# Kernel tuning notes

Measured on AMD Instinct MI355X. Metric: run time of the kernel, lower is better.

Reference implementation:

```python
import jax, jax.numpy as jnp
import numpy as np

H = 64  # lstm_units
FORGET_BIAS = 1.0  # TF LSTMCell default


def setup_inputs() -> dict:
    key = jax.random.key(0)
    k1, k2, k3 = jax.random.split(key, 3)
    B, T = 256, 2048
    x = jax.random.normal(k1, (B, T, 1), dtype=jnp.float32)
    # Layer 1: LSTMCell(64), input dim 1 -> kernel [(1+64), 4*64]
    W1 = jax.random.normal(k2, (1 + H, 4 * H), dtype=jnp.float32) * 0.1
    b1 = jnp.zeros((4 * H,), dtype=jnp.float32)
    # Layer 2: LSTMCell(1), input dim 64 -> kernel [(64+1), 4*1]
    W2 = jax.random.normal(k3, (H + 1, 4), dtype=jnp.float32) * 0.1
    b2 = jnp.zeros((4,), dtype=jnp.float32)
    return {"x": x, "W1": W1, "b1": b1, "W2": W2, "b2": b2}


def _lstm_step(c, h, xt, W, b):
    # TF LSTMCell: gates from concat([x, h]) @ W + b, order i, j, f, o
    z = jnp.concatenate([xt, h], axis=-1) @ W + b
    i, j, f, o = jnp.split(z, 4, axis=-1)
    c_new = jax.nn.sigmoid(f + FORGET_BIAS) * c + jax.nn.sigmoid(i) * jnp.tanh(j)
    h_new = jax.nn.sigmoid(o) * jnpp_tanh(c_new) if False else jax.nn.sigmoid(o) * jnp.tanh(c_new)
    return c_new, h_new


def reference(x, W1, b1, W2, b2):
    # x: [B, T, 1] -> outputs of 2-layer stacked LSTM, final layer size 1
    B = x.shape[0]

    def step(carry, xt):
        c1, h1, c2, h2 = carry
        c1, h1 = _lstm_step(c1, h1, xt, W1, b1)
        c2, h2 = _lstm_step(c2, h2, h1, W2, b2)
        return (c1, h1, c2, h2), h2

    init = (
        jnp.zeros((B, H), x.dtype),
        jnp.zeros((B, H), x.dtype),
        jnp.zeros((B, 1), x.dtype),
        jnp.zeros((B, 1), x.dtype),
    )
    x_tbf = jnp.swapaxes(x, 0, 1)  # [T, B, 1]
    _, ys = jax.lax.scan(step, init, x_tbf)  # ys: [T, B, 1]
    return jnp.swapaxes(ys, 0, 1)  # [B, T, 1]
```

## Files before the change

kernel.cpp:

```cpp
#include <hip/hip_runtime.h>

constexpr int kT = 2048;
constexpr int kB = 256;
constexpr int kH = 64;

__device__ __forceinline__ float fast_sig(float x) {
    return __builtin_amdgcn_rcpf(1.0f + __expf(-x));
}
__device__ __forceinline__ float fast_tanh(float x) {
    float t = __expf(2.0f * x);
    return 1.0f - 2.0f * __builtin_amdgcn_rcpf(t + 1.0f);
}

__global__ __launch_bounds__(320) void lstm2_kernel(
    const float* __restrict__ x, const float* __restrict__ W1,
    const float* __restrict__ b1, const float* __restrict__ W2,
    const float* __restrict__ b2, float* __restrict__ out)
{
    __shared__ float x_lds[kT];
    __shared__ float h1_lds[2][kH];

    const int tid = threadIdx.x;
    const int b = blockIdx.x;
    const float* xg = x + (size_t)b * kT;
    float* outg = out + (size_t)b * kT;

    for (int i = tid; i < kT; i += 320) x_lds[i] = xg[i];
    if (tid < kH) { h1_lds[0][tid] = 0.0f; h1_lds[1][tid] = 0.0f; }

    const int w = tid >> 6;
    const int l = tid & 63;

    float w0 = 0.0f, b1g = 0.0f;
    float wh[kH];
    float c1 = 0.0f;
    int u = 0, g = 0;

    float w2p0 = 0, w2p1 = 0, w2p2 = 0, w2p3 = 0;
    float4 w2t = {0, 0, 0, 0}, b2v = {0, 0, 0, 0};
    float c2 = 0.0f, h2 = 0.0f;
    float zi_s = 0, zj_s = 0, zf_s = 0, zo_s = 0;

    if (w < 4) {
        g = l >> 4;
        u = 16 * w + (l & 15);
        const int col = g * 64 + u;
        w0 = W1[col];
        b1g = b1[col];
        #pragma unroll
        for (int k = 0; k < kH; ++k) wh[k] = W1[(k + 1) * 256 + col];
    } else {
        const int s = l & 15, gg = l >> 4;
        w2p0 = W2[(s +  0) * 4 + gg];
        w2p1 = W2[(s + 16) * 4 + gg];
        w2p2 = W2[(s + 32) * 4 + gg];
        w2p3 = W2[(s + 48) * 4 + gg];
        w2t = ((const float4*)W2)[kH];
        b2v = ((const float4*)b2)[0];
    }
    __syncthreads();

    int cur = 0;
    for (int t = 0; t < kT; ++t) {
        const int nxt = cur ^ 1;
        if (w < 4) {
            const float xt = x_lds[t];
            float z0 = fmaf(xt, w0, b1g), z1 = 0.0f, z2 = 0.0f, z3 = 0.0f;
            const float4* h4 = (const float4*)h1_lds[cur];
            #pragma unroll
            for (int k = 0; k < 16; ++k) {
                float4 h = h4[k];
                z0 = fmaf(h.x, wh[4 * k + 0], z0);
                z1 = fmaf(h.y, wh[4 * k + 1], z1);
                z2 = fmaf(h.z, wh[4 * k + 2], z2);
                z3 = fmaf(h.w, wh[4 * k + 3], z3);
            }
            float z = (z0 + z1) + (z2 + z3);
            float zz = (g == 1) ? 2.0f * z : ((g == 2) ? z + 1.0f : z);
            float sg = fast_sig(zz);
            float a = (g == 1) ? fmaf(2.0f, sg, -1.0f) : sg;
            const int base = l & 15;
            const float ai = __shfl(a, base);
            const float aj = __shfl(a, base + 16);
            const float af = __shfl(a, base + 32);
            const float ao = __shfl(a, base + 48);
            c1 = fmaf(af, c1, ai * aj);
            const float h1n = ao * fast_tanh(c1);
            if (g == 0) h1_lds[nxt][u] = h1n;
        } else {
            if (t >= 2) {
                const float zi = zi_s + h2 * w2t.x;
                const float zj = zj_s + h2 * w2t.y;
                const float zf = zf_s + h2 * w2t.z;
                const float zo = zo_s + h2 * w2t.w;
                c2 = fast_sig(zf + 1.0f) * c2 + fast_sig(zi) * fast_tanh(zj);
                h2 = fast_sig(zo) * fast_tanh(c2);
                if (l == 0) outg[t - 2] = h2;
            }
            if (t >= 1) {
                const int s = l & 15;
                const float* hb = h1_lds[cur];
                float p = hb[s] * w2p0;
                p = fmaf(hb[s + 16], w2p1, p);
                p = fmaf(hb[s + 32], w2p2, p);
                p = fmaf(hb[s + 48], w2p3, p);
                p += __shfl_xor(p, 1);
                p += __shfl_xor(p, 2);
                p += __shfl_xor(p, 4);
                p += __shfl_xor(p, 8);
                zi_s = __shfl(p, s)      + b2v.x;
                zj_s = __shfl(p, s + 16) + b2v.y;
                zf_s = __shfl(p, s + 32) + b2v.z;
                zo_s = __shfl(p, s + 48) + b2v.w;
            }
        }
        __syncthreads();
        cur = nxt;
    }

    if (w == 4) {
        {
            const float zi = zi_s + h2 * w2t.x;
            const float zj = zj_s + h2 * w2t.y;
            const float zf = zf_s + h2 * w2t.z;
            const float zo = zo_s + h2 * w2t.w;
            c2 = fast_sig(zf + 1.0f) * c2 + fast_sig(zi) * fast_tanh(zj);
            h2 = fast_sig(zo) * fast_tanh(c2);
            if (l == 0) outg[kT - 2] = h2;
        }
        {
            const int s = l & 15;
            const float* hb = h1_lds[cur];
            float p = hb[s] * w2p0;
            p = fmaf(hb[s + 16], w2p1, p);
            p = fmaf(hb[s + 32], w2p2, p);
            p = fmaf(hb[s + 48], w2p3, p);
            p += __shfl_xor(p, 1);
            p += __shfl_xor(p, 2);
            p += __shfl_xor(p, 4);
            p += __shfl_xor(p, 8);
            const float zi = __shfl(p, s)      + b2v.x + h2 * w2t.x;
            const float zj = __shfl(p, s + 16) + b2v.y + h2 * w2t.y;
            const float zf = __shfl(p, s + 32) + b2v.z + h2 * w2t.z;
            const float zo = __shfl(p, s + 48) + b2v.w + h2 * w2t.w;
            c2 = fast_sig(zf + 1.0f) * c2 + fast_sig(zi) * fast_tanh(zj);
            h2 = fast_sig(zo) * fast_tanh(c2);
            if (l == 0) outg[kT - 1] = h2;
        }
    }
}

extern "C" void kernel_launch(void* const* d_in, const int* in_sizes, int n_in,
                              void* d_out, int out_size, void* d_ws, size_t ws_size,
                              hipStream_t stream) {
    const float* x  = (const float*)d_in[0];
    const float* W1 = (const float*)d_in[1];
    const float* b1 = (const float*)d_in[2];
    const float* W2 = (const float*)d_in[3];
    const float* b2 = (const float*)d_in[4];
    float* out = (float*)d_out;
    lstm2_kernel<<<kB, 320, 0, stream>>>(x, W1, b1, W2, b2, out);
}
```

Before: 1.134 ms.

## Split layer-1 hidden dot product across two lanes, doubling layer-1 waves

Each layer-1 gate column's 64-element recurrent dot product is now split across two adjacent lanes, each holding 32 weights, and the two halves are combined with a lane shuffle. The block grows from five to nine wavefronts (eight for layer 1, one for layer 2). The goal is to halve the serial FMA chain on the per-timestep critical path and free weight registers. In exchange it adds a shuffle per step, more waves joining each per-step barrier, and more LDS broadcast reads.

```diff
diff --git a/kernel.cpp b/kernel.cpp
--- a/kernel.cpp
+++ b/kernel.cpp
@@ -3,6 +3,7 @@
 constexpr int kT = 2048;
 constexpr int kB = 256;
 constexpr int kH = 64;
+constexpr int kThreads = 576;
 
 __device__ __forceinline__ float fast_sig(float x) {
     return __builtin_amdgcn_rcpf(1.0f + __expf(-x));
@@ -12,7 +13,7 @@
     return 1.0f - 2.0f * __builtin_amdgcn_rcpf(t + 1.0f);
 }
 
-__global__ __launch_bounds__(320) void lstm2_kernel(
+__global__ __launch_bounds__(kThreads) void lstm2_kernel(
     const float* __restrict__ x, const float* __restrict__ W1,
     const float* __restrict__ b1, const float* __restrict__ W2,
     const float* __restrict__ b2, float* __restrict__ out)
@@ -25,30 +26,40 @@
     const float* xg = x + (size_t)b * kT;
     float* outg = out + (size_t)b * kT;
 
-    for (int i = tid; i < kT; i += 320) x_lds[i] = xg[i];
+    for (int i = tid; i < kT; i += kThreads) x_lds[i] = xg[i];
     if (tid < kH) { h1_lds[0][tid] = 0.0f; h1_lds[1][tid] = 0.0f; }
 
     const int w = tid >> 6;
     const int l = tid & 63;
 
     float w0 = 0.0f, b1g = 0.0f;
-    float wh[kH];
+    float4 wq[8];
+    #pragma unroll
+    for (int q = 0; q < 8; ++q) wq[q] = make_float4(0.f, 0.f, 0.f, 0.f);
     float c1 = 0.0f;
-    int u = 0, g = 0;
+    int g = 0, k = 0, hoff = 0;
 
     float w2p0 = 0, w2p1 = 0, w2p2 = 0, w2p3 = 0;
     float4 w2t = {0, 0, 0, 0}, b2v = {0, 0, 0, 0};
     float c2 = 0.0f, h2 = 0.0f;
     float zi_s = 0, zj_s = 0, zf_s = 0, zo_s = 0;
 
-    if (w < 4) {
+    if (w < 8) {
         g = l >> 4;
-        u = 16 * w + (l & 15);
+        const int uw = (l & 15) >> 1;
+        k = l & 1;
+        const int u = 8 * w + uw;
         const int col = g * 64 + u;
+        hoff = 32 * k;
         w0 = W1[col];
         b1g = b1[col];
         #pragma unroll
-        for (int k = 0; k < kH; ++k) wh[k] = W1[(k + 1) * 256 + col];
+        for (int q = 0; q < 8; ++q) {
+            wq[q].x = W1[(32 * k + 4 * q + 1) * 256 + col];
+            wq[q].y = W1[(32 * k + 4 * q + 2) * 256 + col];
+            wq[q].z = W1[(32 * k + 4 * q + 3) * 256 + col];
+            wq[q].w = W1[(32 * k + 4 * q + 4) * 256 + col];
+        }
     } else {
         const int s = l & 15, gg = l >> 4;
         w2p0 = W2[(s +  0) * 4 + gg];
@@ -63,19 +74,21 @@
     int cur = 0;
     for (int t = 0; t < kT; ++t) {
         const int nxt = cur ^ 1;
-        if (w < 4) {
+        if (w < 8) {
             const float xt = x_lds[t];
-            float z0 = fmaf(xt, w0, b1g), z1 = 0.0f, z2 = 0.0f, z3 = 0.0f;
-            const float4* h4 = (const float4*)h1_lds[cur];
+            float z0 = 0.f, z1 = 0.f, z2 = 0.f, z3 = 0.f;
+            const float4* h4 = (const float4*)(&h1_lds[cur][hoff]);
             #pragma unroll
-            for (int k = 0; k < 16; ++k) {
-                float4 h = h4[k];
-                z0 = fmaf(h.x, wh[4 * k + 0], z0);
-                z1 = fmaf(h.y, wh[4 * k + 1], z1);
-                z2 = fmaf(h.z, wh[4 * k + 2], z2);
-                z3 = fmaf(h.w, wh[4 * k + 3], z3);
+            for (int q = 0; q < 8; ++q) {
+                float4 h = h4[q];
+                z0 = fmaf(h.x, wq[q].x, z0);
+                z1 = fmaf(h.y, wq[q].y, z1);
+                z2 = fmaf(h.z, wq[q].z, z2);
+                z3 = fmaf(h.w, wq[q].w, z3);
             }
             float z = (z0 + z1) + (z2 + z3);
+            z += __shfl_xor(z, 1);
+            z += fmaf(xt, w0, b1g);
             float zz = (g == 1) ? 2.0f * z : ((g == 2) ? z + 1.0f : z);
             float sg = fast_sig(zz);
             float a = (g == 1) ? fmaf(2.0f, sg, -1.0f) : sg;
@@ -86,7 +99,8 @@
             const float ao = __shfl(a, base + 48);
             c1 = fmaf(af, c1, ai * aj);
             const float h1n = ao * fast_tanh(c1);
-            if (g == 0) h1_lds[nxt][u] = h1n;
+            if ((l & 0x31) == 0)
+                h1_lds[nxt][8 * w + (l >> 1)] = h1n;
         } else {
             if (t >= 2) {
                 const float zi = zi_s + h2 * w2t.x;
@@ -118,7 +132,7 @@
         cur = nxt;
     }
 
-    if (w == 4) {
+    if (w == 8) {
         {
             const float zi = zi_s + h2 * w2t.x;
             const float zj = zj_s + h2 * w2t.y;
@@ -159,5 +173,5 @@
     const float* W2 = (const float*)d_in[3];
     const float* b2 = (const float*)d_in[4];
     float* out = (float*)d_out;
-    lstm2_kernel<<<kB, 320, 0, stream>>>(x, W1, b1, W2, b2, out);
+    lstm2_kernel<<<kB, kThreads, 0, stream>>>(x, W1, b1, W2, b2, out);
 }
```

Result: slower. 1.212 ms (+6.9%).
